# Optimization experiments

Measured on AMD Instinct MI355X. Metric: run time of the kernel, lower is better.

Reference implementation:

```python
import jax, jax.numpy as jnp
import numpy as np

C_S = 384
C_Z = 128
C_OUT = 1


def setup_inputs() -> dict:
    key = jax.random.key(0)
    k1, k2, k3 = jax.random.split(key, 3)
    B, N = 1, 1024
    s = jax.random.normal(k1, (B, N, C_S), dtype=jnp.float32)
    z = jax.random.normal(k2, (B, N, N, C_Z), dtype=jnp.float32)
    # Linear(2*c_s + c_z -> c_out); init='final' zeros weights in the original,
    # use small random weights for a meaningful correctness baseline.
    W = jax.random.normal(k3, (C_OUT, 2 * C_S + C_Z), dtype=jnp.float32) * 0.02
    b = jnp.zeros((C_OUT,), dtype=jnp.float32)
    return {"s": s, "z": z, "W": W, "b": b}


def reference(s, z, W, b):
    # Mathematically identical to cat([s_i, s_j, z], -1) @ W.T + b, but
    # decomposed so the (B,N,N,2*c_s+c_z) intermediate is never materialized.
    Wi = W[:, :C_S]            # weights hitting s_i (broadcast over j)
    Wj = W[:, C_S:2 * C_S]     # weights hitting s_j (broadcast over i)
    Wz = W[:, 2 * C_S:]        # weights hitting z
    si = jnp.einsum('bnd,od->bno', s, Wi)          # [B,N,c_out]
    sj = jnp.einsum('bnd,od->bno', s, Wj)          # [B,N,c_out]
    zz = jnp.einsum('bnmc,oc->bnmo', z, Wz)        # [B,N,N,c_out]
    logits = si[:, :, None, :] + sj[:, None, :, :] + zz + b
    return logits
```

## Files before the change

### kernel.cpp

```cpp
#include <hip/hip_runtime.h>

#define C_S 384
#define C_Z 128
#define N_SEQ 1024

__global__ __launch_bounds__(256) void sisj_kernel(const float* __restrict__ s,
                                                   const float* __restrict__ W,
                                                   const float* __restrict__ b,
                                                   float* __restrict__ si,
                                                   float* __restrict__ sj) {
    const int lane = threadIdx.x & 63;
    const int wave = threadIdx.x >> 6;
    const int n = blockIdx.x * 4 + wave;

    const float* srow = s + (size_t)n * C_S;
    const float* Wi = W;
    const float* Wj = W + C_S;

    float acc_i = 0.f, acc_j = 0.f;
#pragma unroll
    for (int j = 0; j < C_S / 64; ++j) {
        const int idx = lane + 64 * j;
        const float v = srow[idx];
        acc_i += v * Wi[idx];
        acc_j += v * Wj[idx];
    }
#pragma unroll
    for (int mask = 32; mask >= 1; mask >>= 1) {
        acc_i += __shfl_xor(acc_i, mask);
        acc_j += __shfl_xor(acc_j, mask);
    }
    if (lane == 0) {
        si[n] = acc_i;
        sj[n] = acc_j + b[0];
    }
}

#define U_PAIRS 8
#define CONTACT_BLOCKS 2048

__global__ __launch_bounds__(256) void contact_kernel(const float* __restrict__ z,
                                                      const float* __restrict__ W,
                                                      const float* __restrict__ si,
                                                      const float* __restrict__ sj,
                                                      float* __restrict__ out) {
    const int lane = threadIdx.x & 63;
    const int wave = threadIdx.x >> 6;
    const int half = lane >> 5;
    const int l = lane & 31;
    const int gw = blockIdx.x * 4 + wave;
    const int nwaves = CONTACT_BLOCKS * 4;

    const float4 wz = *(const float4*)(W + 2 * C_S + 4 * l);

    const int NPAIRS = (N_SEQ * N_SEQ) / 2;
    const int NCHUNK = NPAIRS / U_PAIRS;

    for (int c = gw; c < NCHUNK; c += nwaves) {
        const float* zb = z + (size_t)c * (U_PAIRS * 256) + 4 * lane;

        float4 z4[U_PAIRS];
#pragma unroll
        for (int u = 0; u < U_PAIRS; ++u) {
            z4[u] = *(const float4*)(zb + u * 256);
        }

        float p[U_PAIRS];
#pragma unroll
        for (int u = 0; u < U_PAIRS; ++u) {
            p[u] = z4[u].x * wz.x + z4[u].y * wz.y + z4[u].z * wz.z + z4[u].w * wz.w;
        }

#pragma unroll
        for (int mask = 16; mask >= 1; mask >>= 1) {
#pragma unroll
            for (int u = 0; u < U_PAIRS; ++u) {
                p[u] += __shfl_xor(p[u], mask);
            }
        }

        if (l == 0) {
#pragma unroll
            for (int u = 0; u < U_PAIRS; ++u) {
                const long long o = (((long long)c * U_PAIRS + u) << 1) + half;
                const int n = (int)(o >> 10);
                const int m = (int)(o & 1023);
                out[o] = p[u] + si[n] + sj[m];
            }
        }
    }
}

extern "C" void kernel_launch(void* const* d_in, const int* in_sizes, int n_in,
                              void* d_out, int out_size, void* d_ws, size_t ws_size,
                              hipStream_t stream) {
    const float* s = (const float*)d_in[0];
    const float* z = (const float*)d_in[1];
    const float* W = (const float*)d_in[2];
    const float* b = (const float*)d_in[3];
    float* out = (float*)d_out;

    float* si = (float*)d_ws;
    float* sj = si + N_SEQ;

    sisj_kernel<<<N_SEQ / 4, 256, 0, stream>>>(s, W, b, si, sj);

    contact_kernel<<<CONTACT_BLOCKS, 256, 0, stream>>>(z, W, si, sj, out);
}
```

Measured before the change: 683.4 us.

## Fuse si/sj projection into tiled contact kernel with shared-memory row/col terms

Merges the separate si/sj projection kernel into the main contact kernel. Each block now handles a 32x64 tile of (n,m) outputs and first computes its 96 needed si/sj dot products into shared memory. This removes a launch and the workspace round trip. In exchange, each s row's projection is recomputed across many blocks (16x for si, 32x for sj), a barrier is added before the z streaming, and the grid drops from 2048 grid-stride blocks to 512 fixed tiles.

```diff
diff --git a/kernel.cpp b/kernel.cpp
--- a/kernel.cpp
+++ b/kernel.cpp
@@ -4,88 +4,86 @@
 #define C_Z 128
 #define N_SEQ 1024
 
-__global__ __launch_bounds__(256) void sisj_kernel(const float* __restrict__ s,
-                                                   const float* __restrict__ W,
-                                                   const float* __restrict__ b,
-                                                   float* __restrict__ si,
-                                                   float* __restrict__ sj) {
+
+#define TN 32
+#define TM 64
+#define U_PAIRS 8
+
+__global__ __launch_bounds__(256) void fused_contact(const float* __restrict__ s,
+                                                     const float* __restrict__ z,
+                                                     const float* __restrict__ W,
+                                                     const float* __restrict__ b,
+                                                     float* __restrict__ out) {
+    __shared__ float si_l[TN];
+    __shared__ float sj_l[TM];
+
     const int lane = threadIdx.x & 63;
     const int wave = threadIdx.x >> 6;
-    const int n = blockIdx.x * 4 + wave;
 
-    const float* srow = s + (size_t)n * C_S;
-    const float* Wi = W;
-    const float* Wj = W + C_S;
+    const int bid = blockIdx.x;
+    const int n0 = (bid >> 4) * TN;
+    const int m0 = (bid & 15) * TM;
 
-    float acc_i = 0.f, acc_j = 0.f;
+    for (int t = wave * 24; t < wave * 24 + 24; ++t) {
+        const bool is_j = (t >= TN);
+        const int row = is_j ? (m0 + t - TN) : (n0 + t);
+        const float* srow = s + (size_t)row * C_S;
+        const float* Wp = W + (is_j ? C_S : 0);
+        float acc = 0.f;
 #pragma unroll
-    for (int j = 0; j < C_S / 64; ++j) {
-        const int idx = lane + 64 * j;
-        const float v = srow[idx];
-        acc_i += v * Wi[idx];
-        acc_j += v * Wj[idx];
+        for (int d = lane; d < C_S; d += 64) {
+            acc += srow[d] * Wp[d];
+        }
+#pragma unroll
+        for (int mask = 32; mask >= 1; mask >>= 1) {
+            acc += __shfl_xor(acc, mask);
+        }
+        if (lane == 0) {
+            if (is_j) sj_l[t - TN] = acc + b[0];
+            else      si_l[t] = acc;
+        }
     }
-#pragma unroll
-    for (int mask = 32; mask >= 1; mask >>= 1) {
-        acc_i += __shfl_xor(acc_i, mask);
-        acc_j += __shfl_xor(acc_j, mask);
-    }
-    if (lane == 0) {
-        si[n] = acc_i;
-        sj[n] = acc_j + b[0];
-    }
-}
+    __syncthreads();
 
-#define U_PAIRS 8
-#define CONTACT_BLOCKS 2048
-
-__global__ __launch_bounds__(256) void contact_kernel(const float* __restrict__ z,
-                                                      const float* __restrict__ W,
-                                                      const float* __restrict__ si,
-                                                      const float* __restrict__ sj,
-                                                      float* __restrict__ out) {
-    const int lane = threadIdx.x & 63;
-    const int wave = threadIdx.x >> 6;
     const int half = lane >> 5;
     const int l = lane & 31;
-    const int gw = blockIdx.x * 4 + wave;
-    const int nwaves = CONTACT_BLOCKS * 4;
-
     const float4 wz = *(const float4*)(W + 2 * C_S + 4 * l);
 
-    const int NPAIRS = (N_SEQ * N_SEQ) / 2;
-    const int NCHUNK = NPAIRS / U_PAIRS;
+    for (int r = 0; r < 8; ++r) {
+        const int nloc = wave * 8 + r;
+        const int n = n0 + nloc;
+        const float si_v = si_l[nloc];
+        const float* zrow = z + ((size_t)n * N_SEQ + m0) * C_Z;
 
-    for (int c = gw; c < NCHUNK; c += nwaves) {
-        const float* zb = z + (size_t)c * (U_PAIRS * 256) + 4 * lane;
+        for (int c4 = 0; c4 < TM / (2 * U_PAIRS); ++c4) {
+            const float* zb = zrow + c4 * (U_PAIRS * 256) + 4 * lane;
 
-        float4 z4[U_PAIRS];
+            float4 z4[U_PAIRS];
 #pragma unroll
-        for (int u = 0; u < U_PAIRS; ++u) {
-            z4[u] = *(const float4*)(zb + u * 256);
-        }
+            for (int u = 0; u < U_PAIRS; ++u) {
+                z4[u] = *(const float4*)(zb + u * 256);
+            }
 
-        float p[U_PAIRS];
+            float p[U_PAIRS];
 #pragma unroll
-        for (int u = 0; u < U_PAIRS; ++u) {
-            p[u] = z4[u].x * wz.x + z4[u].y * wz.y + z4[u].z * wz.z + z4[u].w * wz.w;
-        }
+            for (int u = 0; u < U_PAIRS; ++u) {
+                p[u] = z4[u].x * wz.x + z4[u].y * wz.y + z4[u].z * wz.z + z4[u].w * wz.w;
+            }
 
 #pragma unroll
-        for (int mask = 16; mask >= 1; mask >>= 1) {
+            for (int mask = 16; mask >= 1; mask >>= 1) {
 #pragma unroll
-            for (int u = 0; u < U_PAIRS; ++u) {
-                p[u] += __shfl_xor(p[u], mask);
+                for (int u = 0; u < U_PAIRS; ++u) {
+                    p[u] += __shfl_xor(p[u], mask);
+                }
             }
-        }
 
-        if (l == 0) {
+            if (l == 0) {
 #pragma unroll
-            for (int u = 0; u < U_PAIRS; ++u) {
-                const long long o = (((long long)c * U_PAIRS + u) << 1) + half;
-                const int n = (int)(o >> 10);
-                const int m = (int)(o & 1023);
-                out[o] = p[u] + si[n] + sj[m];
+                for (int u = 0; u < U_PAIRS; ++u) {
+                    const int mloc = c4 * (2 * U_PAIRS) + 2 * u + half;
+                    out[(size_t)n * N_SEQ + m0 + mloc] = p[u] + si_v + sj_l[mloc];
+                }
             }
         }
     }
@@ -100,10 +98,8 @@
     const float* b = (const float*)d_in[3];
     float* out = (float*)d_out;
 
-    float* si = (float*)d_ws;
-    float* sj = si + N_SEQ;
+    (void)d_ws; (void)ws_size;
 
-    sisj_kernel<<<N_SEQ / 4, 256, 0, stream>>>(s, W, b, si, sj);
-
-    contact_kernel<<<CONTACT_BLOCKS, 256, 0, stream>>>(z, W, si, sj, out);
+    const int blocks = (N_SEQ / TN) * (N_SEQ / TM);
+    fused_contact<<<blocks, 256, 0, stream>>>(s, z, W, b, out);
 }
```

Result: slower. 699.2 us (+2.3%).
